# Kernel optimization log

Measured on AMD Instinct MI355X. Metric: run time of the kernel, lower is better.

## Reference

```python
import jax, jax.numpy as jnp
import numpy as np
from jax import lax

B, T = 256, 256
N_OBS, N_ACT, N_ST = 512, 8, 1024
G, X, P, H = 64, 32, 128, 128
ETA, LAM, KAPPA, RETRIEVE_ITER = 0.4, 0.995, 0.8, 3
OBS_W, MEM_W, ST_W = 1.0, 0.1, 1.0


def setup_inputs() -> dict:
    key = jax.random.key(0)
    ks = jax.random.split(key, 20)
    s = 0.02
    inp = {
        'obs': jax.random.randint(ks[0], (B, T), 0, N_OBS),
        'actions': jax.random.randint(ks[1], (B, T), 0, N_ACT),
        'states': jax.random.randint(ks[2], (B, T), 0, N_ST),
        'obs_emb': jax.random.normal(ks[3], (N_OBS, X)) * s,
        'act_emb': jax.random.normal(ks[4], (N_ACT, G)) * s,
        'g_init': jnp.zeros((G,)),
        'w_ih': jax.random.normal(ks[5], (3 * G, G)) * s,
        'w_hh': jax.random.normal(ks[6], (3 * G, G)) * s,
        'b_ih': jnp.zeros((3 * G,)),
        'b_hh': jnp.zeros((3 * G,)),
        'enc_w1': jax.random.normal(ks[7], (H, G + X)) * s,
        'enc_b1': jnp.zeros((H,)),
        'ln_g': jnp.ones((H,)),
        'ln_b': jnp.zeros((H,)),
        'enc_w2': jax.random.normal(ks[8], (P, H)) * s,
        'enc_b2': jnp.zeros((P,)),
        'dec_obs_w': jax.random.normal(ks[9], (N_OBS, P)) * s,
        'dec_obs_b': jnp.zeros((N_OBS,)),
        'dec_st_w': jax.random.normal(ks[10], (N_ST, P)) * s,
        'dec_st_b': jnp.zeros((N_ST,)),
    }
    return inp


def _l2norm(v, eps=1e-12):
    n = jnp.linalg.norm(v, axis=-1, keepdims=True)
    return v / jnp.maximum(n, eps)


def _gru(x, h, w_ih, w_hh, b_ih, b_hh):
    gi = x @ w_ih.T + b_ih
    gh = h @ w_hh.T + b_hh
    ir, iz, inn = jnp.split(gi, 3, axis=-1)
    hr, hz, hn = jnp.split(gh, 3, axis=-1)
    r = jax.nn.sigmoid(ir + hr)
    z = jax.nn.sigmoid(iz + hz)
    n = jnp.tanh(inn + r * hn)
    return (1.0 - z) * n + z * h


def _forward(obs, actions, states, obs_emb, act_emb, g_init, w_ih, w_hh, b_ih, b_hh,
             enc_w1, enc_b1, ln_g, ln_b, enc_w2, enc_b2,
             dec_obs_w, dec_obs_b, dec_st_w, dec_st_b):
    Bv, Tv = obs.shape
    x_all = obs_emb[obs]      # (B,T,X)
    a_all = act_emb[actions]  # (B,T,G)
    # action used at step t is actions[:, t-1]; step 0 skips the GRU update
    a_prev = jnp.concatenate([jnp.zeros_like(a_all[:, :1]), a_all[:, :-1]], axis=1)

    def step(carry, inps):
        g, M = carry
        t, x, a = inps  # x: (B,X), a: (B,G)
        g = jnp.where(t > 0, _gru(a, g, w_ih, w_hh, b_ih, b_hh), g)
        h = jnp.concatenate([g, x], axis=-1) @ enc_w1.T + enc_b1
        mu = jnp.mean(h, axis=-1, keepdims=True)
        var = jnp.var(h, axis=-1, keepdims=True)
        h = jax.nn.relu((h - mu) / jnp.sqrt(var + 1e-5) * ln_g + ln_b)
        p = jax.nn.relu(h @ enc_w2.T + enc_b2)
        p_norm = _l2norm(p + 1e-6)
        # Hebbian attractor retrieval (fixed small iteration count)
        q = p_norm
        for _ in range(RETRIEVE_ITER):
            q = _l2norm(KAPPA * q + jnp.einsum('bij,bj->bi', M, q))
        p_mem = q
        p_comb = _l2norm(p_norm + p_mem)
        ol = p_comb @ dec_obs_w.T + dec_obs_b
        sl = p_comb @ dec_st_w.T + dec_st_b
        M = LAM * M + ETA * jnp.einsum('bi,bj->bij', p_norm, p_norm)
        return (g, M), (ol, sl, p_norm, p_mem)

    g0 = jnp.broadcast_to(g_init, (Bv, g_init.shape[0]))
    M0 = jnp.zeros((Bv, enc_w2.shape[0], enc_w2.shape[0]), dtype=g_init.dtype)
    ts = jnp.arange(Tv)
    _, (ol, sl, pn, pm) = lax.scan(
        step, (g0, M0), (ts, x_all.transpose(1, 0, 2), a_prev.transpose(1, 0, 2)))
    obs_logits = ol.transpose(1, 0, 2)    # (B,T,N_OBS)
    state_logits = sl.transpose(1, 0, 2)  # (B,T,N_ST)
    p = pn.transpose(1, 0, 2)             # (B,T,P)
    p_mem = pm.transpose(1, 0, 2)

    # loss
    lo = jax.nn.log_softmax(obs_logits, axis=-1)
    loss_obs = -jnp.mean(jnp.take_along_axis(lo, obs[..., None], axis=-1))
    loss_mem = jnp.mean((p_mem[:, 1:] - lax.stop_gradient(p[:, :-1])) ** 2)
    ls = jax.nn.log_softmax(state_logits, axis=-1)
    loss_state = -jnp.mean(jnp.take_along_axis(ls, states[..., None], axis=-1))
    loss = OBS_W * loss_obs + MEM_W * loss_mem + ST_W * loss_state
    return obs_logits, state_logits, p, p_mem, loss


def reference(obs, actions, states, obs_emb, act_emb, g_init, w_ih, w_hh, b_ih, b_hh,
              enc_w1, enc_b1, ln_g, ln_b, enc_w2, enc_b2,
              dec_obs_w, dec_obs_b, dec_st_w, dec_st_b):
    return _forward(obs, actions, states, obs_emb, act_emb, g_init, w_ih, w_hh, b_ih, b_hh,
                    enc_w1, enc_b1, ln_g, ln_b, enc_w2, enc_b2,
                    dec_obs_w, dec_obs_b, dec_st_w, dec_st_b)
```

## Files before the change

### kernel.cpp

```cpp
#include <hip/hip_runtime.h>
#include <hip/hip_bf16.h>

#define Bc 256
#define Tc 256
#define NOBS 512
#define NACT 8
#define NST 1024
#define Gc 64
#define Xc 32
#define Pc 128
#define Hc 128

typedef unsigned short u16;
typedef unsigned int u32;
typedef __attribute__((ext_vector_type(4))) float f32x4;
typedef __attribute__((ext_vector_type(8))) short bf16x8;

__device__ __forceinline__ u16 f2bf(float f) {
    __hip_bfloat16 h = __float2bfloat16(f);
    return __builtin_bit_cast(u16, h);
}
__device__ __forceinline__ float bf2f(u16 v) {
    u32 x = ((u32)v) << 16;
    return __builtin_bit_cast(float, x);
}
__device__ __forceinline__ u32 pack2(float a, float b) {
    return (u32)f2bf(a) | (((u32)f2bf(b)) << 16);
}
__device__ __forceinline__ float dot4(f32x4 a, f32x4 b) {
    return a.x * b.x + a.y * b.y + a.z * b.z + a.w * b.w;
}

template <int CTRL>
__device__ __forceinline__ float dpp_add(float x) {
    int xi = __builtin_bit_cast(int, x);
    int yi = __builtin_amdgcn_update_dpp(0, xi, CTRL, 0xF, 0xF, true);
    return x + __builtin_bit_cast(float, yi);
}

__device__ __forceinline__ void blockReduce2(float& a, float& b, volatile float* red, int tid) {
    a = dpp_add<0x141>(a); b = dpp_add<0x141>(b);
    a = dpp_add<0x140>(a); b = dpp_add<0x140>(b);
    a += __shfl_xor(a, 16, 64); b += __shfl_xor(b, 16, 64);
    a += __shfl_xor(a, 32, 64); b += __shfl_xor(b, 32, 64);
    __syncthreads();
    if ((tid & 63) == 0) { int w = tid >> 6; red[w] = a; red[8 + w] = b; }
    __syncthreads();
    a = ((red[0] + red[1]) + (red[2] + red[3])) + ((red[4] + red[5]) + (red[6] + red[7]));
    b = ((red[8] + red[9]) + (red[10] + red[11])) + ((red[12] + red[13]) + (red[14] + red[15]));
}

__global__ __launch_bounds__(256) void precompute_tabs(
    const float* __restrict__ obs_emb, const float* __restrict__ act_emb,
    const float* __restrict__ w_ih, const float* __restrict__ b_ih,
    const float* __restrict__ enc_w1, const float* __restrict__ enc_b1,
    float* __restrict__ hx_tab, float* __restrict__ gi_tab)
{
    int idx = blockIdx.x * 256 + threadIdx.x;
    if (idx < NOBS * Hc) {
        int o = idx >> 7, rr = idx & 127;
        const f32x4* oe = (const f32x4*)(obs_emb + o * Xc);
        const f32x4* w = (const f32x4*)(enc_w1 + rr * (Gc + Xc) + Gc);
        float s = enc_b1[rr];
#pragma unroll
        for (int j = 0; j < 8; ++j) s += dot4(oe[j], w[j]);
        hx_tab[idx] = s;
    } else if (idx < NOBS * Hc + NACT * 3 * Gc) {
        int k = idx - NOBS * Hc;
        int a = k / 192, row = k - a * 192;
        const f32x4* ae = (const f32x4*)(act_emb + a * Gc);
        const f32x4* w = (const f32x4*)(w_ih + row * Gc);
        float s = b_ih[row];
#pragma unroll
        for (int j = 0; j < 16; ++j) s += dot4(ae[j], w[j]);
        gi_tab[k] = s;
    }
}

__global__ __launch_bounds__(512, 2) void scan_kernel(
    const int* __restrict__ obs, const int* __restrict__ actions,
    const float* __restrict__ g_init,
    const float* __restrict__ w_hh, const float* __restrict__ b_hh,
    const float* __restrict__ enc_w1,
    const float* __restrict__ ln_g, const float* __restrict__ ln_b,
    const float* __restrict__ enc_w2, const float* __restrict__ enc_b2,
    const float* __restrict__ hx_tab, const float* __restrict__ gi_tab,
    float* __restrict__ outP, float* __restrict__ outPM,
    float* __restrict__ accs)
{
    int b = blockIdx.x;
    int tid = threadIdx.x;
    int r = tid >> 2, q = tid & 3;

    __shared__ int obs_lds[Tc];
    __shared__ int act_lds[Tc];
    __shared__ __align__(16) float gitab[NACT * 3 * Gc];
    __shared__ __align__(16) float gx[Gc];
    __shared__ __align__(16) float ghl[3 * Gc];
    __shared__ __align__(16) float bhhs[3 * Gc];
    __shared__ __align__(16) float hv[Hc];
    __shared__ __align__(16) float qA[Pc];
    __shared__ __align__(16) float qB[Pc];
    __shared__ __align__(16) float qC[Pc];
    __shared__ __align__(16) float lngs[Hc];
    __shared__ __align__(16) float lnbs[Hc];
    __shared__ __align__(16) float b2s[Pc];
    __shared__ volatile float red[16];

    if (tid < 256) obs_lds[tid] = obs[b * Tc + tid];
    else           act_lds[tid - 256] = actions[b * Tc + (tid - 256)];
    for (int i = tid; i < NACT * 3 * Gc; i += 512) gitab[i] = gi_tab[i];
    if (tid < 3 * Gc) bhhs[tid] = b_hh[tid];
    if (tid < Hc) { lngs[tid] = ln_g[tid]; lnbs[tid] = ln_b[tid]; b2s[tid] = enc_b2[tid]; }
    if (tid < Gc) gx[tid] = g_init[tid];

    float whh[32];
    if (tid < 384) {
        int row = tid >> 1, hh = tid & 1;
        const f32x4* p = (const f32x4*)(w_hh + row * Gc + hh * 32);
#pragma unroll
        for (int i = 0; i < 8; ++i) ((f32x4*)whh)[i] = p[i];
    }
    float w1r[16];
    {
        const f32x4* p = (const f32x4*)(enc_w1 + r * (Gc + Xc) + q * 16);
#pragma unroll
        for (int i = 0; i < 4; ++i) ((f32x4*)w1r)[i] = p[i];
    }
    float w2r[32];
    {
        const f32x4* p = (const f32x4*)(enc_w2 + r * Hc + q * 32);
#pragma unroll
        for (int i = 0; i < 8; ++i) ((f32x4*)w2r)[i] = p[(i + 2 * q) & 7];
    }

    float Mreg[32];
#pragma unroll
    for (int i = 0; i < 32; ++i) Mreg[i] = 0.f;

    float pnprev = 0.f, lmacc = 0.f;
    __syncthreads();

    float hx = hx_tab[obs_lds[0] * Hc + r];

    for (int t = 0; t < Tc; ++t) {
        int tn = (t + 1 < Tc) ? t + 1 : t;
        float hxn = hx_tab[obs_lds[tn] * Hc + r];
        int ai = (t > 0) ? act_lds[t - 1] : 0;
        if (t > 0 && tid < 384) {
            int row = tid >> 1, hh = tid & 1;
            const f32x4* g4 = (const f32x4*)gx;
            float s2 = 0.f;
#pragma unroll
            for (int m = 0; m < 8; ++m) s2 += dot4(g4[hh * 8 + m], ((const f32x4*)whh)[m]);
            s2 = dpp_add<0xB1>(s2);
            if (hh == 0) ghl[row] = s2 + bhhs[row];
        }
        __syncthreads();

        if (t > 0 && tid < 64) {
            const float* git = gitab + ai * 192;
            float ir = git[tid], iz = git[64 + tid], inn = git[128 + tid];
            float hr = ghl[tid], hz = ghl[64 + tid], hn2 = ghl[128 + tid];
            float rr = 1.f / (1.f + __expf(-(ir + hr)));
            float zz = 1.f / (1.f + __expf(-(iz + hz)));
            float nn = tanhf(inn + rr * hn2);
            gx[tid] = (1.f - zz) * nn + zz * gx[tid];
        }
        __syncthreads();

        float hval;
        {
            const f32x4* g4 = (const f32x4*)gx;
            float s = 0.f;
#pragma unroll
            for (int m = 0; m < 4; ++m) s += dot4(g4[q * 4 + m], ((const f32x4*)w1r)[m]);
            s = dpp_add<0xB1>(s);
            s = dpp_add<0x4E>(s);
            hval = s + hx;
        }
        float s1 = hval, s2 = hval * hval;
        blockReduce2(s1, s2, red, tid);
        float mu = s1 * (1.f / 128.f);
        float var = s2 * (1.f / 128.f) - mu * mu;
        float hn = fmaxf((hval - mu) * rsqrtf(var + 1e-5f) * lngs[r] + lnbs[r], 0.f);
        if (q == 0) hv[r] = hn;
        __syncthreads();

        float pval;
        {
            const f32x4* h4 = (const f32x4*)hv;
            float s = 0.f;
#pragma unroll
            for (int m = 0; m < 8; ++m) {
                s += dot4(h4[q * 8 + ((m + 2 * q) & 7)], ((const f32x4*)w2r)[m]);
            }
            s = dpp_add<0xB1>(s);
            s = dpp_add<0x4E>(s);
            pval = fmaxf(s + b2s[r], 0.f) + 1e-6f;
        }
        if (q == 0) qA[r] = pval;
        __syncthreads();

        float v;
        {
            const f32x4* q4 = (const f32x4*)qA;
            float ss = 0.f;
#pragma unroll
            for (int m = 0; m < 8; ++m)
                ss += dot4(q4[q * 8 + ((m + 2 * q) & 7)], ((const f32x4*)Mreg)[m]);
            ss = dpp_add<0xB1>(ss);
            ss = dpp_add<0x4E>(ss);
            v = 0.8f * pval + ss;
            if (q == 0) qB[r] = v;
        }
        __syncthreads();
        {
            const f32x4* q4 = (const f32x4*)qB;
            float ss = 0.f;
#pragma unroll
            for (int m = 0; m < 8; ++m)
                ss += dot4(q4[q * 8 + ((m + 2 * q) & 7)], ((const f32x4*)Mreg)[m]);
            ss = dpp_add<0xB1>(ss);
            ss = dpp_add<0x4E>(ss);
            v = 0.8f * v + ss;
            if (q == 0) qC[r] = v;
        }
        __syncthreads();
        {
            const f32x4* q4 = (const f32x4*)qC;
            float ss = 0.f;
#pragma unroll
            for (int m = 0; m < 8; ++m)
                ss += dot4(q4[q * 8 + ((m + 2 * q) & 7)], ((const f32x4*)Mreg)[m]);
            ss = dpp_add<0xB1>(ss);
            ss = dpp_add<0x4E>(ss);
            v = 0.8f * v + ss;
        }

        float t1 = pval * pval, t2 = v * v;
        blockReduce2(t1, t2, red, tid);
        float inv_np = 1.f / fmaxf(sqrtf(t1), 1e-12f);
        float inv3 = 1.f / fmaxf(sqrtf(t2), 1e-12f);
        float pn = pval * inv_np;
        float pm = v * inv3;
        size_t rowoff = ((size_t)(b * Tc + t)) << 7;
        if (q == 0) {
            outP[rowoff + r] = pn;
            outPM[rowoff + r] = pm;
            if (t > 0) { float d = pm - pnprev; lmacc += d * d; }
        }
        pnprev = pn;

        {
            float cc = 0.4f * pn * inv_np;
            const f32x4* p4 = (const f32x4*)qA;
#pragma unroll
            for (int m = 0; m < 8; ++m) {
                f32x4 pv = p4[q * 8 + ((m + 2 * q) & 7)];
                f32x4 mm = ((const f32x4*)Mreg)[m];
                mm = 0.995f * mm + cc * pv;
                ((f32x4*)Mreg)[m] = mm;
            }
        }
        hx = hxn;
    }

    float z = lmacc;
    z = dpp_add<0xB1>(z);
    z = dpp_add<0x4E>(z);
    z = dpp_add<0x141>(z);
    z = dpp_add<0x140>(z);
    z += __shfl_xor(z, 16, 64);
    z += __shfl_xor(z, 32, 64);
    __syncthreads();
    if ((tid & 63) == 0) red[tid >> 6] = z;
    __syncthreads();
    if (tid == 0) {
        float s = ((red[0] + red[1]) + (red[2] + red[3])) + ((red[4] + red[5]) + (red[6] + red[7]));
        atomicAdd(&accs[2], s);
    }
}

__global__ __launch_bounds__(256, 2) void dec_gemm(
    const float* __restrict__ pn_, const float* __restrict__ pm_,
    const float* __restrict__ wo, const float* __restrict__ bo,
    const float* __restrict__ wsd, const float* __restrict__ bsd,
    float* __restrict__ outO, float* __restrict__ outS)
{
    __shared__ u16 As[128 * 136];
    __shared__ u16 Bs[128 * 136];
    __shared__ float rnorm[128];
    int cb = blockIdx.x;
    int rowbase = blockIdx.y * 128;
    const float* W; const float* bias; float* out; int Nw; int colbase;
    if (cb < 4) { W = wo; bias = bo; out = outO; Nw = 512; colbase = cb * 128; }
    else        { W = wsd; bias = bsd; out = outS; Nw = 1024; colbase = (cb - 4) * 128; }
    int tid = threadIdx.x;
    for (int i = tid; i < 2048; i += 256) {
        int row = i >> 4, kb = i & 15;
        size_t go = ((size_t)(rowbase + row)) * 128 + kb * 8;
        f32x4 a0 = *(const f32x4*)(pn_ + go);
        f32x4 a1 = *(const f32x4*)(pn_ + go + 4);
        f32x4 m0v = *(const f32x4*)(pm_ + go);
        f32x4 m1v = *(const f32x4*)(pm_ + go + 4);
        f32x4 v0 = a0 + m0v, v1 = a1 + m1v;
        uint4 vv;
        vv.x = pack2(v0.x, v0.y); vv.y = pack2(v0.z, v0.w);
        vv.z = pack2(v1.x, v1.y); vv.w = pack2(v1.z, v1.w);
        *(uint4*)(As + row * 136 + kb * 8) = vv;
        size_t gw = ((size_t)(colbase + row)) * 128 + kb * 8;
        f32x4 w0 = *(const f32x4*)(W + gw);
        f32x4 w1 = *(const f32x4*)(W + gw + 4);
        uint4 wv;
        wv.x = pack2(w0.x, w0.y); wv.y = pack2(w0.z, w0.w);
        wv.z = pack2(w1.x, w1.y); wv.w = pack2(w1.z, w1.w);
        *(uint4*)(Bs + row * 136 + kb * 8) = wv;
    }
    __syncthreads();
    {
        int rr = tid >> 1, hh = tid & 1;
        const u16* rowp = As + rr * 136 + hh * 64;
        float ss = 0.f;
#pragma unroll
        for (int i = 0; i < 64; ++i) { float x = bf2f(rowp[i]); ss += x * x; }
        ss += __shfl_xor(ss, 1, 64);
        if (hh == 0) rnorm[rr] = 1.f / fmaxf(sqrtf(ss), 1e-12f);
    }
    __syncthreads();
    int wv_ = tid >> 6, lane = tid & 63;
    int m0 = (wv_ & 1) * 64, n0 = (wv_ >> 1) * 64;
    int lr = lane & 15, lq = lane >> 4;
    const f32x4 vzero = {0.f, 0.f, 0.f, 0.f};
    f32x4 acc[4][4];
#pragma unroll
    for (int a = 0; a < 4; ++a)
#pragma unroll
        for (int c = 0; c < 4; ++c) acc[a][c] = vzero;
#pragma unroll
    for (int ks = 0; ks < 4; ++ks) {
        bf16x8 af[4], bfr[4];
#pragma unroll
        for (int i = 0; i < 4; ++i) {
            af[i]  = *(const bf16x8*)(As + (m0 + i * 16 + lr) * 136 + ks * 32 + lq * 8);
            bfr[i] = *(const bf16x8*)(Bs + (n0 + i * 16 + lr) * 136 + ks * 32 + lq * 8);
        }
#pragma unroll
        for (int mi = 0; mi < 4; ++mi)
#pragma unroll
            for (int ni = 0; ni < 4; ++ni)
                acc[mi][ni] = __builtin_amdgcn_mfma_f32_16x16x32_bf16(af[mi], bfr[ni], acc[mi][ni], 0, 0, 0);
    }
#pragma unroll
    for (int ni = 0; ni < 4; ++ni) {
        int col = colbase + n0 + ni * 16 + lr;
        float bb = bias[col];
#pragma unroll
        for (int mi = 0; mi < 4; ++mi) {
            int rloc = m0 + mi * 16 + lq * 4;
            int row = rowbase + rloc;
#pragma unroll
            for (int k2 = 0; k2 < 4; ++k2) {
                out[((size_t)(row + k2)) * Nw + col] = acc[mi][ni][k2] * rnorm[rloc + k2] + bb;
            }
        }
    }
}

__global__ __launch_bounds__(256) void loss_rows(
    const float* __restrict__ lo_, const float* __restrict__ ls_,
    const int* __restrict__ obs, const int* __restrict__ states,
    float* __restrict__ accs)
{
    __shared__ float part[8];
    int wv = threadIdx.x >> 6, lane = threadIdx.x & 63;
    float accO = 0.f, accS = 0.f;
    int rowbase = blockIdx.x * 128 + wv * 32;
    for (int i = 0; i < 32; ++i) {
        int row = rowbase + i;
        {
            const float* ro = lo_ + ((size_t)row << 9);
            f32x4 u0 = *(const f32x4*)(ro + lane * 8);
            f32x4 u1 = *(const f32x4*)(ro + lane * 8 + 4);
            float m = fmaxf(fmaxf(fmaxf(u0.x, u0.y), fmaxf(u0.z, u0.w)),
                            fmaxf(fmaxf(u1.x, u1.y), fmaxf(u1.z, u1.w)));
#pragma unroll
            for (int k = 1; k < 64; k <<= 1) m = fmaxf(m, __shfl_xor(m, k, 64));
            float se = __expf(u0.x - m) + __expf(u0.y - m) + __expf(u0.z - m) + __expf(u0.w - m) +
                       __expf(u1.x - m) + __expf(u1.y - m) + __expf(u1.z - m) + __expf(u1.w - m);
#pragma unroll
            for (int k = 1; k < 64; k <<= 1) se += __shfl_xor(se, k, 64);
            float lse = m + __logf(se);
            float xt = ro[obs[row]];
            if (lane == 0) accO += lse - xt;
        }
        {
            const float* rs = ls_ + ((size_t)row << 10);
            f32x4 u0 = *(const f32x4*)(rs + lane * 16);
            f32x4 u1 = *(const f32x4*)(rs + lane * 16 + 4);
            f32x4 u2 = *(const f32x4*)(rs + lane * 16 + 8);
            f32x4 u3 = *(const f32x4*)(rs + lane * 16 + 12);
            float m = fmaxf(fmaxf(fmaxf(u0.x, u0.y), fmaxf(u0.z, u0.w)),
                            fmaxf(fmaxf(u1.x, u1.y), fmaxf(u1.z, u1.w)));
            m = fmaxf(m, fmaxf(fmaxf(fmaxf(u2.x, u2.y), fmaxf(u2.z, u2.w)),
                               fmaxf(fmaxf(u3.x, u3.y), fmaxf(u3.z, u3.w))));
#pragma unroll
            for (int k = 1; k < 64; k <<= 1) m = fmaxf(m, __shfl_xor(m, k, 64));
            float se = __expf(u0.x - m) + __expf(u0.y - m) + __expf(u0.z - m) + __expf(u0.w - m) +
                       __expf(u1.x - m) + __expf(u1.y - m) + __expf(u1.z - m) + __expf(u1.w - m) +
                       __expf(u2.x - m) + __expf(u2.y - m) + __expf(u2.z - m) + __expf(u2.w - m) +
                       __expf(u3.x - m) + __expf(u3.y - m) + __expf(u3.z - m) + __expf(u3.w - m);
#pragma unroll
            for (int k = 1; k < 64; k <<= 1) se += __shfl_xor(se, k, 64);
            float lse = m + __logf(se);
            float xt = rs[states[row]];
            if (lane == 0) accS += lse - xt;
        }
    }
    if (lane == 0) { part[wv] = accO; part[4 + wv] = accS; }
    __syncthreads();
    if (threadIdx.x == 0) {
        atomicAdd(&accs[0], part[0] + part[1] + part[2] + part[3]);
        atomicAdd(&accs[1], part[4] + part[5] + part[6] + part[7]);
    }
}

__global__ void finalize_kernel(const float* __restrict__ accs, float* __restrict__ out_loss)
{
    float lo = accs[0] * (1.f / 65536.f);
    float ls = accs[1] * (1.f / 65536.f);
    float lm = accs[2] * (1.f / (256.f * 255.f * 128.f));
    out_loss[0] = lo + 0.1f * lm + ls;
}

extern "C" void kernel_launch(void* const* d_in, const int* in_sizes, int n_in,
                              void* d_out, int out_size, void* d_ws, size_t ws_size,
                              hipStream_t stream)
{
    const int* obs        = (const int*)d_in[0];
    const int* actions    = (const int*)d_in[1];
    const int* states     = (const int*)d_in[2];
    const float* obs_emb  = (const float*)d_in[3];
    const float* act_emb  = (const float*)d_in[4];
    const float* g_init   = (const float*)d_in[5];
    const float* w_ih     = (const float*)d_in[6];
    const float* w_hh     = (const float*)d_in[7];
    const float* b_ih     = (const float*)d_in[8];
    const float* b_hh     = (const float*)d_in[9];
    const float* enc_w1   = (const float*)d_in[10];
    const float* enc_b1   = (const float*)d_in[11];
    const float* ln_g     = (const float*)d_in[12];
    const float* ln_b     = (const float*)d_in[13];
    const float* enc_w2   = (const float*)d_in[14];
    const float* enc_b2   = (const float*)d_in[15];
    const float* dec_obs_w = (const float*)d_in[16];
    const float* dec_obs_b = (const float*)d_in[17];
    const float* dec_st_w  = (const float*)d_in[18];
    const float* dec_st_b  = (const float*)d_in[19];

    float* out = (float*)d_out;
    float* outO    = out;
    float* outS    = out + (size_t)33554432;
    float* outP    = out + (size_t)100663296;
    float* outPM   = out + (size_t)109051904;
    float* outLoss = out + (size_t)117440512;

    float* hx_tab = outS;
    float* gi_tab = outS + 65536;

    float* accs = (float*)d_ws;

    hipMemsetAsync(d_ws, 0, 64, stream);
    precompute_tabs<<<dim3(262), dim3(256), 0, stream>>>(
        obs_emb, act_emb, w_ih, b_ih, enc_w1, enc_b1, hx_tab, gi_tab);
    scan_kernel<<<dim3(256), dim3(512), 0, stream>>>(
        obs, actions, g_init, w_hh, b_hh,
        enc_w1, ln_g, ln_b, enc_w2, enc_b2, hx_tab, gi_tab, outP, outPM, accs);
    dec_gemm<<<dim3(12, 512), dim3(256), 0, stream>>>(
        outP, outPM, dec_obs_w, dec_obs_b, dec_st_w, dec_st_b, outO, outS);
    loss_rows<<<dim3(512), dim3(256), 0, stream>>>(outO, outS, obs, states, accs);
    finalize_kernel<<<dim3(1), dim3(1), 0, stream>>>(accs, outLoss);
}
```

Measured before the change: 1.640 ms.

## Software-pipeline scan step to overlap next GRU/encoder with retrieval, cut barriers

Restructures the per-timestep scan loop so the next step's GRU update and encoder hidden computation overlap with the current step's memory retrieval iterations. The LayerNorm statistics for the next step are folded into the existing norm reduction through a four-value block reduction. Memory decay is replaced by a running lambda scale, which removes the per-step multiply over M. Together these reduce the number of __syncthreads per step. The loss kernel also gets twice as many blocks with half the rows each. The rescaled memory (clam growing each step) may change floating-point rounding and risks drifting over long sequences.

```diff
diff --git a/kernel.cpp b/kernel.cpp
--- a/kernel.cpp
+++ b/kernel.cpp
@@ -48,6 +48,26 @@
     __syncthreads();
     a = ((red[0] + red[1]) + (red[2] + red[3])) + ((red[4] + red[5]) + (red[6] + red[7]));
     b = ((red[8] + red[9]) + (red[10] + red[11])) + ((red[12] + red[13]) + (red[14] + red[15]));
+}
+
+__device__ __forceinline__ void blockReduce4(float& a, float& b, float& c, float& d,
+                                             volatile float* red, int tid) {
+    a = dpp_add<0x141>(a); b = dpp_add<0x141>(b); c = dpp_add<0x141>(c); d = dpp_add<0x141>(d);
+    a = dpp_add<0x140>(a); b = dpp_add<0x140>(b); c = dpp_add<0x140>(c); d = dpp_add<0x140>(d);
+    a += __shfl_xor(a, 16, 64); b += __shfl_xor(b, 16, 64);
+    c += __shfl_xor(c, 16, 64); d += __shfl_xor(d, 16, 64);
+    a += __shfl_xor(a, 32, 64); b += __shfl_xor(b, 32, 64);
+    c += __shfl_xor(c, 32, 64); d += __shfl_xor(d, 32, 64);
+    __syncthreads();
+    if ((tid & 63) == 0) {
+        int w = tid >> 6;
+        red[w] = a; red[8 + w] = b; red[16 + w] = c; red[24 + w] = d;
+    }
+    __syncthreads();
+    a = ((red[0] + red[1]) + (red[2] + red[3])) + ((red[4] + red[5]) + (red[6] + red[7]));
+    b = ((red[8] + red[9]) + (red[10] + red[11])) + ((red[12] + red[13]) + (red[14] + red[15]));
+    c = ((red[16] + red[17]) + (red[18] + red[19])) + ((red[20] + red[21]) + (red[22] + red[23]));
+    d = ((red[24] + red[25]) + (red[26] + red[27])) + ((red[28] + red[29]) + (red[30] + red[31]));
 }
 
 __global__ __launch_bounds__(256) void precompute_tabs(
@@ -105,7 +125,7 @@
     __shared__ __align__(16) float lngs[Hc];
     __shared__ __align__(16) float lnbs[Hc];
     __shared__ __align__(16) float b2s[Pc];
-    __shared__ volatile float red[16];
+    __shared__ volatile float red[32];
 
     if (tid < 256) obs_lds[tid] = obs[b * Tc + tid];
     else           act_lds[tid - 256] = actions[b * Tc + (tid - 256)];
@@ -139,15 +159,49 @@
     for (int i = 0; i < 32; ++i) Mreg[i] = 0.f;
 
     float pnprev = 0.f, lmacc = 0.f;
-    __syncthreads();
-
-    float hx = hx_tab[obs_lds[0] * Hc + r];
+    float lam = 1.f;
+    float clam = 0.4f / 0.995f;
+    const float clam_step = 1.00502513f;
+
+    __syncthreads();
+
+    {
+        float hx0 = hx_tab[obs_lds[0] * Hc + r];
+        const f32x4* g4 = (const f32x4*)gx;
+        float s = 0.f;
+#pragma unroll
+        for (int m = 0; m < 4; ++m) s += dot4(g4[q * 4 + m], ((const f32x4*)w1r)[m]);
+        s = dpp_add<0xB1>(s);
+        s = dpp_add<0x4E>(s);
+        float hval = s + hx0;
+        float s1 = hval, s2 = hval * hval;
+        blockReduce2(s1, s2, red, tid);
+        float mu = s1 * (1.f / 128.f);
+        float var = s2 * (1.f / 128.f) - mu * mu;
+        float hn = fmaxf((hval - mu) * rsqrtf(var + 1e-5f) * lngs[r] + lnbs[r], 0.f);
+        if (q == 0) hv[r] = hn;
+    }
+    __syncthreads();
 
     for (int t = 0; t < Tc; ++t) {
-        int tn = (t + 1 < Tc) ? t + 1 : t;
+        bool more = (t < Tc - 1);
+        int tn = more ? t + 1 : t;
         float hxn = hx_tab[obs_lds[tn] * Hc + r];
-        int ai = (t > 0) ? act_lds[t - 1] : 0;
-        if (t > 0 && tid < 384) {
+        int ai = act_lds[t];
+
+        float pval;
+        {
+            const f32x4* h4 = (const f32x4*)hv;
+            float s = 0.f;
+#pragma unroll
+            for (int m = 0; m < 8; ++m)
+                s += dot4(h4[q * 8 + ((m + 2 * q) & 7)], ((const f32x4*)w2r)[m]);
+            s = dpp_add<0xB1>(s);
+            s = dpp_add<0x4E>(s);
+            pval = fmaxf(s + b2s[r], 0.f) + 1e-6f;
+        }
+        if (q == 0) qA[r] = pval;
+        if (more && tid < 384) {
             int row = tid >> 1, hh = tid & 1;
             const f32x4* g4 = (const f32x4*)gx;
             float s2 = 0.f;
@@ -158,7 +212,19 @@
         }
         __syncthreads();
 
-        if (t > 0 && tid < 64) {
+        float v1;
+        {
+            const f32x4* q4 = (const f32x4*)qA;
+            float ss = 0.f;
+#pragma unroll
+            for (int m = 0; m < 8; ++m)
+                ss += dot4(q4[q * 8 + ((m + 2 * q) & 7)], ((const f32x4*)Mreg)[m]);
+            ss = dpp_add<0xB1>(ss);
+            ss = dpp_add<0x4E>(ss);
+            v1 = 0.8f * pval + lam * ss;
+            if (q == 0) qB[r] = v1;
+        }
+        if (more && tid < 64) {
             const float* git = gitab + ai * 192;
             float ir = git[tid], iz = git[64 + tid], inn = git[128 + tid];
             float hr = ghl[tid], hz = ghl[64 + tid], hn2 = ghl[128 + tid];
@@ -169,77 +235,43 @@
         }
         __syncthreads();
 
-        float hval;
-        {
-            const f32x4* g4 = (const f32x4*)gx;
-            float s = 0.f;
-#pragma unroll
-            for (int m = 0; m < 4; ++m) s += dot4(g4[q * 4 + m], ((const f32x4*)w1r)[m]);
-            s = dpp_add<0xB1>(s);
-            s = dpp_add<0x4E>(s);
-            hval = s + hx;
-        }
-        float s1 = hval, s2 = hval * hval;
-        blockReduce2(s1, s2, red, tid);
-        float mu = s1 * (1.f / 128.f);
-        float var = s2 * (1.f / 128.f) - mu * mu;
-        float hn = fmaxf((hval - mu) * rsqrtf(var + 1e-5f) * lngs[r] + lnbs[r], 0.f);
-        if (q == 0) hv[r] = hn;
-        __syncthreads();
-
-        float pval;
-        {
-            const f32x4* h4 = (const f32x4*)hv;
-            float s = 0.f;
-#pragma unroll
-            for (int m = 0; m < 8; ++m) {
-                s += dot4(h4[q * 8 + ((m + 2 * q) & 7)], ((const f32x4*)w2r)[m]);
-            }
-            s = dpp_add<0xB1>(s);
-            s = dpp_add<0x4E>(s);
-            pval = fmaxf(s + b2s[r], 0.f) + 1e-6f;
-        }
-        if (q == 0) qA[r] = pval;
-        __syncthreads();
-
-        float v;
-        {
-            const f32x4* q4 = (const f32x4*)qA;
+        float v2;
+        {
+            const f32x4* q4 = (const f32x4*)qB;
             float ss = 0.f;
 #pragma unroll
             for (int m = 0; m < 8; ++m)
                 ss += dot4(q4[q * 8 + ((m + 2 * q) & 7)], ((const f32x4*)Mreg)[m]);
             ss = dpp_add<0xB1>(ss);
             ss = dpp_add<0x4E>(ss);
-            v = 0.8f * pval + ss;
-            if (q == 0) qB[r] = v;
+            v2 = 0.8f * v1 + lam * ss;
+            if (q == 0) qC[r] = v2;
+        }
+        float hval2 = 0.f;
+        if (more) {
+            const f32x4* g4 = (const f32x4*)gx;
+            float s = 0.f;
+#pragma unroll
+            for (int m = 0; m < 4; ++m) s += dot4(g4[q * 4 + m], ((const f32x4*)w1r)[m]);
+            s = dpp_add<0xB1>(s);
+            s = dpp_add<0x4E>(s);
+            hval2 = s + hxn;
         }
         __syncthreads();
-        {
-            const f32x4* q4 = (const f32x4*)qB;
+
+        float v;
+        {
+            const f32x4* q4 = (const f32x4*)qC;
             float ss = 0.f;
 #pragma unroll
             for (int m = 0; m < 8; ++m)
                 ss += dot4(q4[q * 8 + ((m + 2 * q) & 7)], ((const f32x4*)Mreg)[m]);
             ss = dpp_add<0xB1>(ss);
             ss = dpp_add<0x4E>(ss);
-            v = 0.8f * v + ss;
-            if (q == 0) qC[r] = v;
-        }
-        __syncthreads();
-        {
-            const f32x4* q4 = (const f32x4*)qC;
-            float ss = 0.f;
-#pragma unroll
-            for (int m = 0; m < 8; ++m)
-                ss += dot4(q4[q * 8 + ((m + 2 * q) & 7)], ((const f32x4*)Mreg)[m]);
-            ss = dpp_add<0xB1>(ss);
-            ss = dpp_add<0x4E>(ss);
-            v = 0.8f * v + ss;
-        }
-
-        float t1 = pval * pval, t2 = v * v;
-        blockReduce2(t1, t2, red, tid);
+            v = 0.8f * v2 + lam * ss;
+        }
+        float t1 = pval * pval, t2 = v * v, t3 = hval2, t4 = hval2 * hval2;
+        blockReduce4(t1, t2, t3, t4, red, tid);
         float inv_np = 1.f / fmaxf(sqrtf(t1), 1e-12f);
         float inv3 = 1.f / fmaxf(sqrtf(t2), 1e-12f);
         float pn = pval * inv_np;
@@ -251,19 +283,26 @@
             if (t > 0) { float d = pm - pnprev; lmacc += d * d; }
         }
         pnprev = pn;
-
-        {
-            float cc = 0.4f * pn * inv_np;
+        {
+            float cc = clam * pn * inv_np;
             const f32x4* p4 = (const f32x4*)qA;
 #pragma unroll
             for (int m = 0; m < 8; ++m) {
                 f32x4 pv = p4[q * 8 + ((m + 2 * q) & 7)];
                 f32x4 mm = ((const f32x4*)Mreg)[m];
-                mm = 0.995f * mm + cc * pv;
+                mm = mm + cc * pv;
                 ((f32x4*)Mreg)[m] = mm;
             }
         }
-        hx = hxn;
+        if (more) {
+            float mu = t3 * (1.f / 128.f);
+            float var = t4 * (1.f / 128.f) - mu * mu;
+            float hn2 = fmaxf((hval2 - mu) * rsqrtf(var + 1e-5f) * lngs[r] + lnbs[r], 0.f);
+            if (q == 0) hv[r] = hn2;
+        }
+        lam *= 0.995f;
+        clam *= clam_step;
+        __syncthreads();
     }
 
     float z = lmacc;
@@ -375,8 +414,8 @@
     __shared__ float part[8];
     int wv = threadIdx.x >> 6, lane = threadIdx.x & 63;
     float accO = 0.f, accS = 0.f;
-    int rowbase = blockIdx.x * 128 + wv * 32;
-    for (int i = 0; i < 32; ++i) {
+    int rowbase = blockIdx.x * 64 + wv * 16;
+    for (int i = 0; i < 16; ++i) {
         int row = rowbase + i;
         {
             const float* ro = lo_ + ((size_t)row << 9);
@@ -478,6 +517,6 @@
         enc_w1, ln_g, ln_b, enc_w2, enc_b2, hx_tab, gi_tab, outP, outPM, accs);
     dec_gemm<<<dim3(12, 512), dim3(256), 0, stream>>>(
         outP, outPM, dec_obs_w, dec_obs_b, dec_st_w, dec_st_b, outO, outS);
-    loss_rows<<<dim3(512), dim3(256), 0, stream>>>(outO, outS, obs, states, accs);
+    loss_rows<<<dim3(1024), dim3(256), 0, stream>>>(outO, outS, obs, states, accs);
     finalize_kernel<<<dim3(1), dim3(1), 0, stream>>>(accs, outLoss);
 }
```

Measured after the change: 1.994 ms. 21.6% more time.
